# Kernel optimization log

Measured on AMD Instinct MI355X. Metric: run time of the kernel, lower is better.

Reference implementation:

```python
import jax, jax.numpy as jnp
import numpy as np

VOCAB, D, T, NC = 21128, 768, 4, 10
B, S = 64, 512


def setup_inputs() -> dict:
    key = jax.random.key(0)
    ks = jax.random.split(key, 12)
    inv = 1.0 / np.sqrt(D)
    return {
        "words": jax.random.randint(ks[0], (B, S), 0, VOCAB),
        "target": jax.random.randint(ks[1], (B, S), 0, T),
        "corpus": jax.random.randint(ks[2], (B,), 0, NC),
        "embed_table": jax.random.normal(ks[3], (VOCAB, D), jnp.float32) * 0.02,
        "shared_W": jax.random.uniform(ks[4], (D, T), jnp.float32, -inv, inv),
        "shared_b": jax.random.uniform(ks[5], (T,), jnp.float32, -inv, inv),
        "domain_A": jax.random.uniform(ks[6], (NC, D, T), jnp.float32, -inv, inv),
        "domain_b": jax.random.uniform(ks[7], (NC, T), jnp.float32, -inv, inv),
        "trans_m": jax.random.normal(ks[8], (T, T), jnp.float32) * 0.1,
        "start_scores": jax.random.normal(ks[9], (T,), jnp.float32) * 0.1,
        "end_scores": jax.random.normal(ks[10], (T,), jnp.float32) * 0.1,
    }


def reference(words, target, corpus, embed_table, shared_W, shared_b,
              domain_A, domain_b, trans_m, start_scores, end_scores):
    mask = words != 0                                    # (B,S) pad mask
    x = embed_table[words]                               # (B,S,D) embedding lookup
    # domain-gated projection: shared linear + per-corpus bmm
    out1 = jnp.einsum('bsd,dt->bst', x, shared_W) + shared_b
    A = domain_A[corpus]                                 # (B,D,T)
    bb = domain_b[corpus][:, None, :]                    # (B,1,T)
    out2 = jnp.einsum('bsd,bdt->bst', x, A) + bb
    logits = jax.nn.log_softmax(out1 + out2, axis=-1)    # (B,S,T)

    # --- CRF normalizer (forward algorithm, logsumexp scan over time) ---
    alpha0 = logits[:, 0] + start_scores[None, :]        # (B,T)

    def step(alpha, inp):
        logit_t, m_t = inp                               # (B,T), (B,)
        tmp = alpha[:, :, None] + logit_t[:, None, :] + trans_m[None, :, :]
        new = jax.nn.logsumexp(tmp, axis=1)              # (B,T)
        return jnp.where(m_t[:, None], new, alpha), None

    xs = (jnp.swapaxes(logits[:, 1:], 0, 1), jnp.swapaxes(mask[:, 1:], 0, 1))
    alpha, _ = jax.lax.scan(step, alpha0, xs)
    normalizer = jax.nn.logsumexp(alpha + end_scores[None, :], axis=1)  # (B,)

    # --- gold path score ---
    emit = jnp.take_along_axis(logits, target[..., None], axis=-1)[..., 0]  # (B,S)
    emit = jnp.where(mask, emit, 0.0)
    tr = trans_m[target[:, :-1], target[:, 1:]]          # (B,S-1)
    tr = jnp.where(mask[:, 1:], tr, 0.0)
    last_idx = jnp.maximum(jnp.sum(mask.astype(jnp.int32), axis=1) - 1, 0)
    bidx = jnp.arange(words.shape[0])
    gold = (emit.sum(1) + tr.sum(1)
            + start_scores[target[:, 0]]
            + end_scores[target[bidx, last_idx]])
    return normalizer - gold                             # (B,) NLL per sequence
```

## Files before the change

### kernel.cpp

```cpp
#include <hip/hip_runtime.h>

#define NB 64
#define NS 512
#define ND 768
#define NT 4
#define NC 10
#define NEG (-1e30f)

__global__ __launch_bounds__(256) void logits_phaseA_kernel(
    const int* __restrict__ words, const int* __restrict__ target,
    const int* __restrict__ corpus, const float* __restrict__ embed,
    const float* __restrict__ sW, const float* __restrict__ sb,
    const float* __restrict__ dA, const float* __restrict__ db,
    const float* __restrict__ trans,
    float4* __restrict__ chunkM,
    float*  __restrict__ partG,
    int*    __restrict__ partC,
    float4* __restrict__ l0ws)
{
  __shared__ float wt[NT][ND];
  __shared__ float4 bl;
  __shared__ float4 lsm[16];

  const int tid = threadIdx.x;
  const int blk = blockIdx.x;
  const int b = blk >> 5;
  const int j = blk & 31;

  const int c = __builtin_amdgcn_readfirstlane(corpus[b]);
  const float4* sW4 = (const float4*)sW;
  const float4* dA4 = ((const float4*)dA) + (size_t)c * ND;
#pragma unroll
  for (int k = 0; k < 3; ++k) {
    const int d = tid + k * 256;
    const float4 a = sW4[d];
    const float4 e = dA4[d];
    wt[0][d] = a.x + e.x;
    wt[1][d] = a.y + e.y;
    wt[2][d] = a.z + e.z;
    wt[3][d] = a.w + e.w;
  }
  if (tid == 0) {
    const float4 a = *(const float4*)sb;
    const float4 e = ((const float4*)db)[c];
    bl = make_float4(a.x + e.x, a.y + e.y, a.z + e.z, a.w + e.w);
  }
  __syncthreads();

  const int grp = tid >> 4;
  const int q   = tid & 15;
  const int g   = blk * 16 + grp;

  const float4* __restrict__ row4 = (const float4*)(embed + (size_t)words[g] * ND);
  const float4* __restrict__ Wt4 = (const float4*)&wt[0][0];

  float4 x[12];
#pragma unroll
  for (int i = 0; i < 12; ++i) x[i] = row4[i * 16 + q];

  float a0 = 0.f, a1 = 0.f, a2 = 0.f, a3 = 0.f;
#pragma unroll
  for (int i = 0; i < 12; ++i) {
    const float4 w0 = Wt4[0 * 192 + i * 16 + q];
    const float4 w1 = Wt4[1 * 192 + i * 16 + q];
    const float4 w2 = Wt4[2 * 192 + i * 16 + q];
    const float4 w3 = Wt4[3 * 192 + i * 16 + q];
    a0 = fmaf(x[i].x, w0.x, a0); a0 = fmaf(x[i].y, w0.y, a0);
    a0 = fmaf(x[i].z, w0.z, a0); a0 = fmaf(x[i].w, w0.w, a0);
    a1 = fmaf(x[i].x, w1.x, a1); a1 = fmaf(x[i].y, w1.y, a1);
    a1 = fmaf(x[i].z, w1.z, a1); a1 = fmaf(x[i].w, w1.w, a1);
    a2 = fmaf(x[i].x, w2.x, a2); a2 = fmaf(x[i].y, w2.y, a2);
    a2 = fmaf(x[i].z, w2.z, a2); a2 = fmaf(x[i].w, w2.w, a2);
    a3 = fmaf(x[i].x, w3.x, a3); a3 = fmaf(x[i].y, w3.y, a3);
    a3 = fmaf(x[i].z, w3.z, a3); a3 = fmaf(x[i].w, w3.w, a3);
  }

#pragma unroll
  for (int off = 8; off; off >>= 1) {
    a0 += __shfl_xor(a0, off, 16);
    a1 += __shfl_xor(a1, off, 16);
    a2 += __shfl_xor(a2, off, 16);
    a3 += __shfl_xor(a3, off, 16);
  }

  if (q == 0) {
    a0 += bl.x; a1 += bl.y; a2 += bl.z; a3 += bl.w;
    const float m = fmaxf(fmaxf(a0, a1), fmaxf(a2, a3));
    const float sum = __expf(a0 - m) + __expf(a1 - m) +
                      __expf(a2 - m) + __expf(a3 - m);
    const float lse = m + __logf(sum);
    lsm[grp] = make_float4(a0 - lse, a1 - lse, a2 - lse, a3 - lse);
  }
  __syncthreads();

  if (tid < 16) {
    const int s = j * 16 + tid;
    float gp = 0.f; int cp = 0;
    if (words[b * NS + s] != 0) {
      const int t = target[b * NS + s];
      const float4 lv = lsm[tid];
      gp = (t == 0) ? lv.x : (t == 1) ? lv.y : (t == 2) ? lv.z : lv.w;
      if (s > 0) gp += trans[target[b * NS + s - 1] * 4 + t];
      cp = 1;
    }
#pragma unroll
    for (int off = 8; off; off >>= 1) {
      gp += __shfl_xor(gp, off, 16);
      cp += __shfl_xor(cp, off, 16);
    }
    if (tid == 0) { partG[b * 32 + j] = gp; partC[b * 32 + j] = cp; }
    if (tid == 0 && j == 0) l0ws[b] = lsm[0];
  }

  if (tid >= 64 && tid < 72) {
    const int k = (tid - 64) >> 2;
    const int a = tid & 3;
    const int cg = j * 2 + k;
    const int s_beg = (cg == 0) ? 1 : cg * 8;
    const int s_end = cg * 8 + 8;

    float T[4][4];
#pragma unroll
    for (int i = 0; i < 4; ++i)
#pragma unroll
      for (int t = 0; t < 4; ++t) T[i][t] = trans[i * 4 + t];

    float v0 = (a == 0) ? 0.f : NEG;
    float v1 = (a == 1) ? 0.f : NEG;
    float v2 = (a == 2) ? 0.f : NEG;
    float v3 = (a == 3) ? 0.f : NEG;
    for (int s = s_beg; s < s_end; ++s) {
      if (words[b * NS + s] != 0) {
        const float4 l = lsm[s - j * 16];
        float t0, t1, t2, t3, m, sm;
        float n0, n1, n2, n3;
        t0 = v0 + T[0][0]; t1 = v1 + T[1][0]; t2 = v2 + T[2][0]; t3 = v3 + T[3][0];
        m = fmaxf(fmaxf(t0, t1), fmaxf(t2, t3));
        sm = __expf(t0 - m) + __expf(t1 - m) + __expf(t2 - m) + __expf(t3 - m);
        n0 = m + __logf(sm) + l.x;
        t0 = v0 + T[0][1]; t1 = v1 + T[1][1]; t2 = v2 + T[2][1]; t3 = v3 + T[3][1];
        m = fmaxf(fmaxf(t0, t1), fmaxf(t2, t3));
        sm = __expf(t0 - m) + __expf(t1 - m) + __expf(t2 - m) + __expf(t3 - m);
        n1 = m + __logf(sm) + l.y;
        t0 = v0 + T[0][2]; t1 = v1 + T[1][2]; t2 = v2 + T[2][2]; t3 = v3 + T[3][2];
        m = fmaxf(fmaxf(t0, t1), fmaxf(t2, t3));
        sm = __expf(t0 - m) + __expf(t1 - m) + __expf(t2 - m) + __expf(t3 - m);
        n2 = m + __logf(sm) + l.z;
        t0 = v0 + T[0][3]; t1 = v1 + T[1][3]; t2 = v2 + T[2][3]; t3 = v3 + T[3][3];
        m = fmaxf(fmaxf(t0, t1), fmaxf(t2, t3));
        sm = __expf(t0 - m) + __expf(t1 - m) + __expf(t2 - m) + __expf(t3 - m);
        n3 = m + __logf(sm) + l.w;
        v0 = n0; v1 = n1; v2 = n2; v3 = n3;
      }
    }
    chunkM[(size_t)(b * 64 + cg) * 4 + a] = make_float4(v0, v1, v2, v3);
  }
}

__global__ __launch_bounds__(256) void crf_tree_kernel(
    const int* __restrict__ target, const float* __restrict__ start_s,
    const float* __restrict__ end_s, const float4* __restrict__ chunkM,
    const float* __restrict__ partG, const int* __restrict__ partC,
    const float4* __restrict__ l0ws, float* __restrict__ out)
{
  __shared__ float bufA[64][16];
  __shared__ float bufB[32][16];
  __shared__ float goldS;
  __shared__ int   cntS;

  const int tid = threadIdx.x;
  const int b = blockIdx.x;

  {
    const int cc = tid >> 2, a = tid & 3;
    const float4 v = chunkM[(size_t)(b * 64 + cc) * 4 + a];
    bufA[cc][a * 4 + 0] = v.x;
    bufA[cc][a * 4 + 1] = v.y;
    bufA[cc][a * 4 + 2] = v.z;
    bufA[cc][a * 4 + 3] = v.w;
  }

  if (tid < 32) {
    float g = partG[b * 32 + tid];
    int   cp = partC[b * 32 + tid];
#pragma unroll
    for (int off = 16; off; off >>= 1) {
      g  += __shfl_xor(g, off, 32);
      cp += __shfl_xor(cp, off, 32);
    }
    if (tid == 0) { goldS = g; cntS = cp; }
  }

  float* src = &bufA[0][0];
  float* dst = &bufB[0][0];
  for (int n = 64; n > 1; n >>= 1) {
    const int entries = (n >> 1) * 16;
    __syncthreads();
    for (int e = tid; e < entries; e += 256) {
      const int p = e >> 4;
      const int aa = (e >> 2) & 3;
      const int jj = e & 3;
      const float* C1 = src + (2 * p) * 16;
      const float* C2 = src + (2 * p + 1) * 16;
      const float t0 = C1[aa * 4 + 0] + C2[0 * 4 + jj];
      const float t1 = C1[aa * 4 + 1] + C2[1 * 4 + jj];
      const float t2 = C1[aa * 4 + 2] + C2[2 * 4 + jj];
      const float t3 = C1[aa * 4 + 3] + C2[3 * 4 + jj];
      const float m = fmaxf(fmaxf(t0, t1), fmaxf(t2, t3));
      dst[p * 16 + aa * 4 + jj] =
          m + __logf(__expf(t0 - m) + __expf(t1 - m) +
                     __expf(t2 - m) + __expf(t3 - m));
    }
    float* tmp = src; src = dst; dst = tmp;
  }
  __syncthreads();

  if (tid == 0) {
    const float* C = &bufA[0][0];
    const float4 l0 = l0ws[b];
    const float a0 = l0.x + start_s[0];
    const float a1 = l0.y + start_s[1];
    const float a2 = l0.z + start_s[2];
    const float a3 = l0.w + start_s[3];
    float af[4];
#pragma unroll
    for (int jj = 0; jj < 4; ++jj) {
      const float t0 = a0 + C[0 * 4 + jj];
      const float t1 = a1 + C[1 * 4 + jj];
      const float t2 = a2 + C[2 * 4 + jj];
      const float t3 = a3 + C[3 * 4 + jj];
      const float m = fmaxf(fmaxf(t0, t1), fmaxf(t2, t3));
      af[jj] = m + __logf(__expf(t0 - m) + __expf(t1 - m) +
                          __expf(t2 - m) + __expf(t3 - m));
    }
    const float z0 = af[0] + end_s[0], z1 = af[1] + end_s[1];
    const float z2 = af[2] + end_s[2], z3 = af[3] + end_s[3];
    const float mz = fmaxf(fmaxf(z0, z1), fmaxf(z2, z3));
    const float norm = mz + __logf(__expf(z0 - mz) + __expf(z1 - mz) +
                                   __expf(z2 - mz) + __expf(z3 - mz));

    const int last = (cntS - 1) > 0 ? (cntS - 1) : 0;
    const float gold = goldS + start_s[target[b * NS]] + end_s[target[b * NS + last]];
    out[b] = norm - gold;
  }
}

extern "C" void kernel_launch(void* const* d_in, const int* in_sizes, int n_in,
                              void* d_out, int out_size, void* d_ws, size_t ws_size,
                              hipStream_t stream) {
  const int*   words   = (const int*)d_in[0];
  const int*   target  = (const int*)d_in[1];
  const int*   corpus  = (const int*)d_in[2];
  const float* embed   = (const float*)d_in[3];
  const float* sW      = (const float*)d_in[4];
  const float* sb      = (const float*)d_in[5];
  const float* dA      = (const float*)d_in[6];
  const float* db      = (const float*)d_in[7];
  const float* trans   = (const float*)d_in[8];
  const float* start_s = (const float*)d_in[9];
  const float* end_s   = (const float*)d_in[10];
  float* out = (float*)d_out;

  float4* chunkM = (float4*)d_ws;
  float4* l0ws   = chunkM + (size_t)NB * 64 * 4;
  float*  partG  = (float*)(l0ws + NB);
  int*    partC  = (int*)(partG + NB * 32);

  logits_phaseA_kernel<<<NB * 32, 256, 0, stream>>>(
      words, target, corpus, embed, sW, sb, dA, db, trans,
      chunkM, partG, partC, l0ws);
  crf_tree_kernel<<<NB, 256, 0, stream>>>(
      target, start_s, end_s, chunkM, partG, partC, l0ws, out);
}
```

Measured before the change: 33.69 us.

## Split fused logits and CRF chunk pass into separate kernels

The single kernel that computed log-softmax logits and then ran the gold-score partials and the 8-step CRF chunk scan is split in two. The logits kernel now only computes logits and writes them to a workspace buffer. A new 128-thread kernel reads them back, forms gold and count partials and runs the chunk scans, with each thread's logits and mask loads hoisted into registers. The goal is to take the serial, few-thread CRF tail and its extra barrier off the memory-bound embedding blocks, and to drop the up-front x register array. The cost is an extra kernel launch and a global write and read of the logits tensor.

```diff
diff --git a/kernel.cpp b/kernel.cpp
--- a/kernel.cpp
+++ b/kernel.cpp
@@ -7,27 +7,20 @@
 #define NC 10
 #define NEG (-1e30f)
 
-__global__ __launch_bounds__(256) void logits_phaseA_kernel(
-    const int* __restrict__ words, const int* __restrict__ target,
-    const int* __restrict__ corpus, const float* __restrict__ embed,
-    const float* __restrict__ sW, const float* __restrict__ sb,
-    const float* __restrict__ dA, const float* __restrict__ db,
-    const float* __restrict__ trans,
-    float4* __restrict__ chunkM,
-    float*  __restrict__ partG,
-    int*    __restrict__ partC,
-    float4* __restrict__ l0ws)
+__global__ __launch_bounds__(256) void logits_kernel(
+    const int* __restrict__ words, const int* __restrict__ corpus,
+    const float* __restrict__ embed, const float* __restrict__ sW,
+    const float* __restrict__ sb, const float* __restrict__ dA,
+    const float* __restrict__ db, float* __restrict__ logits)
 {
   __shared__ float wt[NT][ND];
   __shared__ float4 bl;
-  __shared__ float4 lsm[16];
 
   const int tid = threadIdx.x;
   const int blk = blockIdx.x;
   const int b = blk >> 5;
-  const int j = blk & 31;
-
   const int c = __builtin_amdgcn_readfirstlane(corpus[b]);
+
   const float4* sW4 = (const float4*)sW;
   const float4* dA4 = ((const float4*)dA) + (size_t)c * ND;
 #pragma unroll
@@ -54,33 +47,30 @@
   const float4* __restrict__ row4 = (const float4*)(embed + (size_t)words[g] * ND);
   const float4* __restrict__ Wt4 = (const float4*)&wt[0][0];
 
-  float4 x[12];
-#pragma unroll
-  for (int i = 0; i < 12; ++i) x[i] = row4[i * 16 + q];
-
   float a0 = 0.f, a1 = 0.f, a2 = 0.f, a3 = 0.f;
 #pragma unroll
   for (int i = 0; i < 12; ++i) {
+    const float4 xv = row4[i * 16 + q];
     const float4 w0 = Wt4[0 * 192 + i * 16 + q];
     const float4 w1 = Wt4[1 * 192 + i * 16 + q];
     const float4 w2 = Wt4[2 * 192 + i * 16 + q];
     const float4 w3 = Wt4[3 * 192 + i * 16 + q];
-    a0 = fmaf(x[i].x, w0.x, a0); a0 = fmaf(x[i].y, w0.y, a0);
-    a0 = fmaf(x[i].z, w0.z, a0); a0 = fmaf(x[i].w, w0.w, a0);
-    a1 = fmaf(x[i].x, w1.x, a1); a1 = fmaf(x[i].y, w1.y, a1);
-    a1 = fmaf(x[i].z, w1.z, a1); a1 = fmaf(x[i].w, w1.w, a1);
-    a2 = fmaf(x[i].x, w2.x, a2); a2 = fmaf(x[i].y, w2.y, a2);
-    a2 = fmaf(x[i].z, w2.z, a2); a2 = fmaf(x[i].w, w2.w, a2);
-    a3 = fmaf(x[i].x, w3.x, a3); a3 = fmaf(x[i].y, w3.y, a3);
-    a3 = fmaf(x[i].z, w3.z, a3); a3 = fmaf(x[i].w, w3.w, a3);
+    a0 = fmaf(xv.x, w0.x, a0); a0 = fmaf(xv.y, w0.y, a0);
+    a0 = fmaf(xv.z, w0.z, a0); a0 = fmaf(xv.w, w0.w, a0);
+    a1 = fmaf(xv.x, w1.x, a1); a1 = fmaf(xv.y, w1.y, a1);
+    a1 = fmaf(xv.z, w1.z, a1); a1 = fmaf(xv.w, w1.w, a1);
+    a2 = fmaf(xv.x, w2.x, a2); a2 = fmaf(xv.y, w2.y, a2);
+    a2 = fmaf(xv.z, w2.z, a2); a2 = fmaf(xv.w, w2.w, a2);
+    a3 = fmaf(xv.x, w3.x, a3); a3 = fmaf(xv.y, w3.y, a3);
+    a3 = fmaf(xv.z, w3.z, a3); a3 = fmaf(xv.w, w3.w, a3);
   }
 
 #pragma unroll
   for (int off = 8; off; off >>= 1) {
-    a0 += __shfl_xor(a0, off, 16);
-    a1 += __shfl_xor(a1, off, 16);
-    a2 += __shfl_xor(a2, off, 16);
-    a3 += __shfl_xor(a3, off, 16);
+    a0 += __shfl_xor(a0, off);
+    a1 += __shfl_xor(a1, off);
+    a2 += __shfl_xor(a2, off);
+    a3 += __shfl_xor(a3, off);
   }
 
   if (q == 0) {
@@ -89,79 +79,102 @@
     const float sum = __expf(a0 - m) + __expf(a1 - m) +
                       __expf(a2 - m) + __expf(a3 - m);
     const float lse = m + __logf(sum);
-    lsm[grp] = make_float4(a0 - lse, a1 - lse, a2 - lse, a3 - lse);
-  }
-  __syncthreads();
-
-  if (tid < 16) {
-    const int s = j * 16 + tid;
-    float gp = 0.f; int cp = 0;
-    if (words[b * NS + s] != 0) {
-      const int t = target[b * NS + s];
-      const float4 lv = lsm[tid];
-      gp = (t == 0) ? lv.x : (t == 1) ? lv.y : (t == 2) ? lv.z : lv.w;
-      if (s > 0) gp += trans[target[b * NS + s - 1] * 4 + t];
-      cp = 1;
-    }
-#pragma unroll
-    for (int off = 8; off; off >>= 1) {
-      gp += __shfl_xor(gp, off, 16);
-      cp += __shfl_xor(cp, off, 16);
-    }
-    if (tid == 0) { partG[b * 32 + j] = gp; partC[b * 32 + j] = cp; }
-    if (tid == 0 && j == 0) l0ws[b] = lsm[0];
-  }
-
-  if (tid >= 64 && tid < 72) {
-    const int k = (tid - 64) >> 2;
-    const int a = tid & 3;
-    const int cg = j * 2 + k;
-    const int s_beg = (cg == 0) ? 1 : cg * 8;
-    const int s_end = cg * 8 + 8;
-
-    float T[4][4];
-#pragma unroll
-    for (int i = 0; i < 4; ++i)
-#pragma unroll
-      for (int t = 0; t < 4; ++t) T[i][t] = trans[i * 4 + t];
-
-    float v0 = (a == 0) ? 0.f : NEG;
-    float v1 = (a == 1) ? 0.f : NEG;
-    float v2 = (a == 2) ? 0.f : NEG;
-    float v3 = (a == 3) ? 0.f : NEG;
-    for (int s = s_beg; s < s_end; ++s) {
-      if (words[b * NS + s] != 0) {
-        const float4 l = lsm[s - j * 16];
-        float t0, t1, t2, t3, m, sm;
-        float n0, n1, n2, n3;
-        t0 = v0 + T[0][0]; t1 = v1 + T[1][0]; t2 = v2 + T[2][0]; t3 = v3 + T[3][0];
-        m = fmaxf(fmaxf(t0, t1), fmaxf(t2, t3));
-        sm = __expf(t0 - m) + __expf(t1 - m) + __expf(t2 - m) + __expf(t3 - m);
-        n0 = m + __logf(sm) + l.x;
-        t0 = v0 + T[0][1]; t1 = v1 + T[1][1]; t2 = v2 + T[2][1]; t3 = v3 + T[3][1];
-        m = fmaxf(fmaxf(t0, t1), fmaxf(t2, t3));
-        sm = __expf(t0 - m) + __expf(t1 - m) + __expf(t2 - m) + __expf(t3 - m);
-        n1 = m + __logf(sm) + l.y;
-        t0 = v0 + T[0][2]; t1 = v1 + T[1][2]; t2 = v2 + T[2][2]; t3 = v3 + T[3][2];
-        m = fmaxf(fmaxf(t0, t1), fmaxf(t2, t3));
-        sm = __expf(t0 - m) + __expf(t1 - m) + __expf(t2 - m) + __expf(t3 - m);
-        n2 = m + __logf(sm) + l.z;
-        t0 = v0 + T[0][3]; t1 = v1 + T[1][3]; t2 = v2 + T[2][3]; t3 = v3 + T[3][3];
-        m = fmaxf(fmaxf(t0, t1), fmaxf(t2, t3));
-        sm = __expf(t0 - m) + __expf(t1 - m) + __expf(t2 - m) + __expf(t3 - m);
-        n3 = m + __logf(sm) + l.w;
-        v0 = n0; v1 = n1; v2 = n2; v3 = n3;
-      }
-    }
-    chunkM[(size_t)(b * 64 + cg) * 4 + a] = make_float4(v0, v1, v2, v3);
-  }
+    ((float4*)logits)[g] = make_float4(a0 - lse, a1 - lse, a2 - lse, a3 - lse);
+  }
+}
+
+__global__ __launch_bounds__(128) void crf_phaseA_kernel(
+    const int* __restrict__ words, const int* __restrict__ target,
+    const float* __restrict__ trans, const float* __restrict__ logits,
+    float4* __restrict__ chunkM,
+    float*  __restrict__ partG,
+    int*    __restrict__ partC)
+{
+  const int tid = threadIdx.x;
+  const int b = blockIdx.x >> 1;
+  const int h = blockIdx.x & 1;
+
+  const float* lg = logits + (size_t)b * NS * NT;
+  const int* wb = words + b * NS;
+  const int* tb = target + b * NS;
+
+  float gp = 0.f; int cp = 0;
+#pragma unroll
+  for (int qq = 0; qq < 2; ++qq) {
+    const int s = h * 256 + tid * 2 + qq;
+    if (wb[s] != 0) {
+      const int t = tb[s];
+      gp += lg[s * 4 + t];
+      if (s > 0) gp += trans[tb[s - 1] * 4 + t];
+      ++cp;
+    }
+  }
+#pragma unroll
+  for (int off = 32; off; off >>= 1) {
+    gp += __shfl_xor(gp, off);
+    cp += __shfl_xor(cp, off);
+  }
+  if ((tid & 63) == 0) {
+    partG[(b * 2 + h) * 2 + (tid >> 6)] = gp;
+    partC[(b * 2 + h) * 2 + (tid >> 6)] = cp;
+  }
+
+  const int cg = h * 32 + (tid >> 2);
+  const int a = tid & 3;
+  const int s_beg = (cg == 0) ? 1 : cg * 8;
+  const int s_end = cg * 8 + 8;
+
+  float T[4][4];
+#pragma unroll
+  for (int i = 0; i < 4; ++i)
+#pragma unroll
+    for (int j = 0; j < 4; ++j) T[i][j] = trans[i * 4 + j];
+
+  float4 lv[8]; int wm[8];
+#pragma unroll
+  for (int qq = 0; qq < 8; ++qq) {
+    const int s = cg * 8 + qq;
+    wm[qq] = (s >= s_beg) ? wb[s] : 0;
+    lv[qq] = *(const float4*)(lg + s * 4);
+  }
+
+  float v0 = (a == 0) ? 0.f : NEG;
+  float v1 = (a == 1) ? 0.f : NEG;
+  float v2 = (a == 2) ? 0.f : NEG;
+  float v3 = (a == 3) ? 0.f : NEG;
+#pragma unroll
+  for (int qq = 0; qq < 8; ++qq) {
+    if (wm[qq] != 0) {
+      const float4 l = lv[qq];
+      float t0, t1, t2, t3, m, sm;
+      float n0, n1, n2, n3;
+      t0 = v0 + T[0][0]; t1 = v1 + T[1][0]; t2 = v2 + T[2][0]; t3 = v3 + T[3][0];
+      m = fmaxf(fmaxf(t0, t1), fmaxf(t2, t3));
+      sm = __expf(t0 - m) + __expf(t1 - m) + __expf(t2 - m) + __expf(t3 - m);
+      n0 = m + __logf(sm) + l.x;
+      t0 = v0 + T[0][1]; t1 = v1 + T[1][1]; t2 = v2 + T[2][1]; t3 = v3 + T[3][1];
+      m = fmaxf(fmaxf(t0, t1), fmaxf(t2, t3));
+      sm = __expf(t0 - m) + __expf(t1 - m) + __expf(t2 - m) + __expf(t3 - m);
+      n1 = m + __logf(sm) + l.y;
+      t0 = v0 + T[0][2]; t1 = v1 + T[1][2]; t2 = v2 + T[2][2]; t3 = v3 + T[3][2];
+      m = fmaxf(fmaxf(t0, t1), fmaxf(t2, t3));
+      sm = __expf(t0 - m) + __expf(t1 - m) + __expf(t2 - m) + __expf(t3 - m);
+      n2 = m + __logf(sm) + l.z;
+      t0 = v0 + T[0][3]; t1 = v1 + T[1][3]; t2 = v2 + T[2][3]; t3 = v3 + T[3][3];
+      m = fmaxf(fmaxf(t0, t1), fmaxf(t2, t3));
+      sm = __expf(t0 - m) + __expf(t1 - m) + __expf(t2 - m) + __expf(t3 - m);
+      n3 = m + __logf(sm) + l.w;
+      v0 = n0; v1 = n1; v2 = n2; v3 = n3;
+    }
+  }
+  chunkM[(size_t)(b * 64 + cg) * 4 + a] = make_float4(v0, v1, v2, v3);
 }
 
 __global__ __launch_bounds__(256) void crf_tree_kernel(
     const int* __restrict__ target, const float* __restrict__ start_s,
     const float* __restrict__ end_s, const float4* __restrict__ chunkM,
     const float* __restrict__ partG, const int* __restrict__ partC,
-    const float4* __restrict__ l0ws, float* __restrict__ out)
+    const float* __restrict__ logits, float* __restrict__ out)
 {
   __shared__ float bufA[64][16];
   __shared__ float bufB[32][16];
@@ -180,13 +193,13 @@
     bufA[cc][a * 4 + 3] = v.w;
   }
 
-  if (tid < 32) {
-    float g = partG[b * 32 + tid];
-    int   cp = partC[b * 32 + tid];
-#pragma unroll
-    for (int off = 16; off; off >>= 1) {
-      g  += __shfl_xor(g, off, 32);
-      cp += __shfl_xor(cp, off, 32);
+  if (tid < 4) {
+    float g  = partG[b * 4 + tid];
+    int   cp = partC[b * 4 + tid];
+#pragma unroll
+    for (int off = 2; off; off >>= 1) {
+      g  += __shfl_xor(g, off, 4);
+      cp += __shfl_xor(cp, off, 4);
     }
     if (tid == 0) { goldS = g; cntS = cp; }
   }
@@ -217,7 +230,7 @@
 
   if (tid == 0) {
     const float* C = &bufA[0][0];
-    const float4 l0 = l0ws[b];
+    const float4 l0 = *(const float4*)(logits + (size_t)b * NS * NT);
     const float a0 = l0.x + start_s[0];
     const float a1 = l0.y + start_s[1];
     const float a2 = l0.z + start_s[2];
@@ -261,14 +274,15 @@
   const float* end_s   = (const float*)d_in[10];
   float* out = (float*)d_out;
 
-  float4* chunkM = (float4*)d_ws;
-  float4* l0ws   = chunkM + (size_t)NB * 64 * 4;
-  float*  partG  = (float*)(l0ws + NB);
-  int*    partC  = (int*)(partG + NB * 32);
-
-  logits_phaseA_kernel<<<NB * 32, 256, 0, stream>>>(
-      words, target, corpus, embed, sW, sb, dA, db, trans,
-      chunkM, partG, partC, l0ws);
-  crf_tree_kernel<<<NB, 256, 0, stream>>>(
-      target, start_s, end_s, chunkM, partG, partC, l0ws, out);
-}
+  float*  logits = (float*)d_ws;
+  float4* chunkM = (float4*)(logits + (size_t)NB * NS * NT);
+  float*  partG  = (float*)(chunkM + (size_t)NB * 64 * 4);
+  int*    partC  = (int*)(partG + NB * 4);
+
+  logits_kernel<<<NB * 32, 256, 0, stream>>>(words, corpus, embed, sW, sb,
+                                             dA, db, logits);
+  crf_phaseA_kernel<<<NB * 2, 128, 0, stream>>>(words, target, trans, logits,
+                                                chunkM, partG, partC);
+  crf_tree_kernel<<<NB, 256, 0, stream>>>(target, start_s, end_s, chunkM,
+                                          partG, partC, logits, out);
+}
```

Measured after the change: 31.82 us. 5.5% less time.
